# Kernel tuning notes

Hardware: AMD Instinct MI355X
Metric: run time of the kernel (lower is better)

Reference implementation:

```python
import jax, jax.numpy as jnp
import numpy as np

N = 100000
D = 128
E = 1600000
NUM_STEPS = 8
LAM0 = 1.0
LAM1 = 1.0
ALPHA = 1.0 / (1.0 + 0.0 + LAM0 + LAM1)  # args.alp == 0 path


def setup_inputs() -> dict:
    key = jax.random.key(0)
    ks = jax.random.split(key, 12)
    X = jax.random.normal(ks[0], (N, D), dtype=jnp.float32)
    # H init: normal(0, 1/in_features) + I  (notresidual=False branch)
    H1 = jax.random.normal(ks[1], (D, D), dtype=jnp.float32) * (1.0 / D) + jnp.eye(D, dtype=jnp.float32)
    H2 = jax.random.normal(ks[2], (D, D), dtype=jnp.float32) * (1.0 / D) + jnp.eye(D, dtype=jnp.float32)
    w_beta = jax.random.uniform(ks[3], (E,), dtype=jnp.float32)
    w_gamma = jax.random.uniform(ks[4], (E,), dtype=jnp.float32)
    d_beta = jax.random.uniform(ks[5], (N,), dtype=jnp.float32)
    d_gamma = jax.random.uniform(ks[6], (N,), dtype=jnp.float32)
    src_beta = jax.random.randint(ks[7], (E,), 0, N, dtype=jnp.int32)
    dst_beta = jax.random.randint(ks[8], (E,), 0, N, dtype=jnp.int32)
    src_gamma = jax.random.randint(ks[9], (E,), 0, N, dtype=jnp.int32)
    dst_gamma = jax.random.randint(ks[10], (E,), 0, N, dtype=jnp.int32)
    return {"X": X, "H1": H1, "H2": H2, "w_beta": w_beta, "w_gamma": w_gamma,
            "d_beta": d_beta, "d_gamma": d_gamma,
            "src_beta": src_beta, "dst_beta": dst_beta,
            "src_gamma": src_gamma, "dst_gamma": dst_gamma}


def _spmm(w, src, dst, Y):
    # (sparse A) @ Y with A[dst, src] = w
    return jax.ops.segment_sum(w[:, None] * Y[src], dst, num_segments=N)


def reference(X, H1, H2, w_beta, w_gamma, d_beta, d_gamma,
              src_beta, dst_beta, src_gamma, dst_gamma):
    # Q_tild = lam0*D_beta + lam1*D_gamma + I  (diagonal)
    q = LAM0 * d_beta + LAM1 * d_gamma + 1.0  # [N]
    S1 = H1 + H1.T
    P1 = H1 @ H1.T
    S2 = H2 + H2.T
    P2 = H2 @ H2.T
    Y0 = X
    Y = X
    for _ in range(NUM_STEPS):
        AbY = _spmm(w_beta, src_beta, dst_beta, Y)    # A_beta @ Y
        AgY = _spmm(w_gamma, src_gamma, dst_gamma, Y)  # A_gamma @ Y
        term_beta = AbY @ S1 - d_beta[:, None] * (Y @ P1)
        # L_gamma @ Y = D_gamma@Y - A_gamma@Y
        term_gamma = (d_gamma[:, None] * Y - AgY
                      + AgY @ S2 - d_gamma[:, None] * (Y @ P2))
        Y_hat = LAM0 * term_beta + Y0 + LAM1 * term_gamma
        Y = (1.0 - ALPHA) * Y + ALPHA * (Y_hat / q[:, None])
    return Y
```

## Files before the change

kernel.cpp:

```cpp
#include <hip/hip_runtime.h>
#include <cstdint>
#include <cstddef>

#define DD 128
#define ATS 68
#define WTS 130

typedef float f32x8 __attribute__((ext_vector_type(8)));


__global__ void count2_k(const int* __restrict__ dstb, const int* __restrict__ dstg,
                         int* __restrict__ degb, int* __restrict__ degg, int E, int gE) {
    int b = blockIdx.x;
    const int* dst = (b < gE) ? dstb : dstg;
    int* deg = (b < gE) ? degb : degg;
    int i = ((b < gE) ? b : b - gE) * blockDim.x + threadIdx.x;
    if (i < E) atomicAdd(&deg[dst[i]], 1);
}

__global__ __launch_bounds__(1024) void scan2_k(const int* __restrict__ degb,
                                                const int* __restrict__ degg,
                                                int* __restrict__ rpb, int* __restrict__ rpg,
                                                int* __restrict__ curb, int* __restrict__ curg,
                                                int n) {
    const int* deg = (blockIdx.x == 0) ? degb : degg;
    int* rp = (blockIdx.x == 0) ? rpb : rpg;
    int* cur = (blockIdx.x == 0) ? curb : curg;
    __shared__ int sums[1024];
    int tid = threadIdx.x;
    int per = (n + 1023) >> 10;
    int start = tid * per;
    int end = min(start + per, n);
    int s = 0;
    for (int i = start; i < end; ++i) s += deg[i];
    sums[tid] = s;
    __syncthreads();
    for (int off = 1; off < 1024; off <<= 1) {
        int v = (tid >= off) ? sums[tid - off] : 0;
        __syncthreads();
        sums[tid] += v;
        __syncthreads();
    }
    int pre = (tid == 0) ? 0 : sums[tid - 1];
    for (int i = start; i < end; ++i) {
        rp[i] = pre;
        cur[i] = pre;
        pre += deg[i];
    }
    if (end == n) rp[n] = pre;
}

__global__ void fill2_k(const int* __restrict__ srcb, const int* __restrict__ dstb,
                        const float* __restrict__ wb,
                        const int* __restrict__ srcg, const int* __restrict__ dstg,
                        const float* __restrict__ wg,
                        int* __restrict__ curb, int* __restrict__ curg,
                        int2* __restrict__ eb, int2* __restrict__ eg, int E, int gE) {
    int b = blockIdx.x;
    bool isb = (b < gE);
    const int* src = isb ? srcb : srcg;
    const int* dst = isb ? dstb : dstg;
    const float* w = isb ? wb : wg;
    int* cur = isb ? curb : curg;
    int2* edges = isb ? eb : eg;
    int i = (isb ? b : b - gE) * blockDim.x + threadIdx.x;
    if (i < E) {
        int d = dst[i];
        int pos = atomicAdd(&cur[d], 1);
        edges[pos] = make_int2(src[i], __float_as_int(w[i]));
    }
}


__global__ __launch_bounds__(256) void prep_k(const float* __restrict__ H,
                                              float* __restrict__ P,
                                              float* __restrict__ S, int sub_ident) {
    int idx = blockIdx.x * 256 + threadIdx.x;
    int i = idx >> 7, j = idx & 127;
    float acc = 0.f;
    for (int k = 0; k < DD; ++k) acc += H[i * DD + k] * H[j * DD + k];
    P[idx] = acc;
    float s = H[i * DD + j] + H[j * DD + i];
    if (sub_ident && i == j) s -= 1.0f;
    S[idx] = s;
}


__global__ void aq_k(const float* __restrict__ db, const float* __restrict__ dg,
                     float* __restrict__ aq, int n) {
    int i = blockIdx.x * blockDim.x + threadIdx.x;
    if (i < n) aq[i] = (1.0f / 3.0f) / (db[i] + dg[i] + 1.0f);
}


__global__ __launch_bounds__(1024, 2) void denseY_k(
    const float* __restrict__ Yc, const float* __restrict__ X,
    const float* __restrict__ db, const float* __restrict__ dg,
    const float* __restrict__ P1, const float* __restrict__ P2,
    const float* __restrict__ S1, const float* __restrict__ S2m,
    float* __restrict__ YS1, float* __restrict__ YSg, float* __restrict__ R, int n)
{
    __shared__ float At[DD * ATS];

    const int tid  = threadIdx.x;
    const int lane = tid & 63;
    const int wid  = tid >> 6;
    const int cw   = wid << 3;
    const int c0   = __builtin_amdgcn_readfirstlane(cw);
    const int row0 = blockIdx.x * 64;
    const int rowc = min(row0 + lane, n - 1);

    {
        const float* gp = Yc + (size_t)rowc * DD + cw;
        float4 v0 = *reinterpret_cast<const float4*>(gp);
        float4 v1 = *reinterpret_cast<const float4*>(gp + 4);
        At[(cw + 0) * ATS + lane] = v0.x;
        At[(cw + 1) * ATS + lane] = v0.y;
        At[(cw + 2) * ATS + lane] = v0.z;
        At[(cw + 3) * ATS + lane] = v0.w;
        At[(cw + 4) * ATS + lane] = v1.x;
        At[(cw + 5) * ATS + lane] = v1.y;
        At[(cw + 6) * ATS + lane] = v1.z;
        At[(cw + 7) * ATS + lane] = v1.w;
    }
    __syncthreads();

    const float dbv = db[rowc];
    const float dgv = dg[rowc];

    float a1[8], a2[8], aR[8];
    {
        const float* xp = X + (size_t)rowc * DD + cw;
        float4 x0 = *reinterpret_cast<const float4*>(xp);
        float4 x1 = *reinterpret_cast<const float4*>(xp + 4);
        float xv[8] = {x0.x, x0.y, x0.z, x0.w, x1.x, x1.y, x1.z, x1.w};
#pragma unroll
        for (int j = 0; j < 8; ++j) {
            a1[j] = 0.f; a2[j] = 0.f;
            aR[j] = xv[j] + dgv * At[(c0 + j) * ATS + lane];
        }
    }

    {
        const f32x8* pS1 = reinterpret_cast<const f32x8*>(S1 + c0);
        const f32x8* pS2 = reinterpret_cast<const f32x8*>(S2m + c0);
        const f32x8* pP1 = reinterpret_cast<const f32x8*>(P1 + c0);
        const f32x8* pP2 = reinterpret_cast<const f32x8*>(P2 + c0);
#pragma unroll 2
        for (int k = 0; k < DD; ++k) {
            f32x8 b1 = pS1[k * 16];
            f32x8 b2 = pS2[k * 16];
            f32x8 b3 = pP1[k * 16];
            f32x8 b4 = pP2[k * 16];
            float a = At[k * ATS + lane];
            float am1 = dbv * a;
            float am2 = dgv * a;
#pragma unroll
            for (int j = 0; j < 8; ++j) {
                a1[j] += a * b1[j];
                a2[j] += a * b2[j];
                aR[j] -= am1 * b3[j] + am2 * b4[j];
            }
        }
    }

    float* W = At;
    const int r2 = tid >> 4;
    const int c2 = (tid & 15) << 3;
    const int row2 = row0 + r2;

    __syncthreads();
#pragma unroll
    for (int j = 0; j < 8; ++j) W[lane * WTS + cw + j] = a1[j];
    __syncthreads();
    if (row2 < n) {
        float ov[8];
#pragma unroll
        for (int j = 0; j < 8; ++j) ov[j] = W[r2 * WTS + c2 + j];
        float* op = YS1 + (size_t)row2 * DD + c2;
        *reinterpret_cast<float4*>(op) = make_float4(ov[0], ov[1], ov[2], ov[3]);
        *reinterpret_cast<float4*>(op + 4) = make_float4(ov[4], ov[5], ov[6], ov[7]);
    }
    __syncthreads();
#pragma unroll
    for (int j = 0; j < 8; ++j) W[lane * WTS + cw + j] = a2[j];
    __syncthreads();
    if (row2 < n) {
        float ov[8];
#pragma unroll
        for (int j = 0; j < 8; ++j) ov[j] = W[r2 * WTS + c2 + j];
        float* op = YSg + (size_t)row2 * DD + c2;
        *reinterpret_cast<float4*>(op) = make_float4(ov[0], ov[1], ov[2], ov[3]);
        *reinterpret_cast<float4*>(op + 4) = make_float4(ov[4], ov[5], ov[6], ov[7]);
    }
    __syncthreads();
#pragma unroll
    for (int j = 0; j < 8; ++j) W[lane * WTS + cw + j] = aR[j];
    __syncthreads();
    if (row2 < n) {
        float ov[8];
#pragma unroll
        for (int j = 0; j < 8; ++j) ov[j] = W[r2 * WTS + c2 + j];
        float* op = R + (size_t)row2 * DD + c2;
        *reinterpret_cast<float4*>(op) = make_float4(ov[0], ov[1], ov[2], ov[3]);
        *reinterpret_cast<float4*>(op + 4) = make_float4(ov[4], ov[5], ov[6], ov[7]);
    }
}


__global__ __launch_bounds__(256, 8) void spmmF_k(
    const int* __restrict__ rpb, const int2* __restrict__ eb,
    const int* __restrict__ rpg, const int2* __restrict__ eg,
    const float* __restrict__ YS1, const float* __restrict__ YSg,
    const float* __restrict__ Yc, const float* __restrict__ R,
    const float* __restrict__ aq,
    float* __restrict__ Yn, int n)
{
    int node = blockIdx.x * 4 + (threadIdx.x >> 6);
    if (node >= n) return;
    int lane = threadIdx.x & 63;

    int jb = rpb[node], be = rpb[node + 1];
    int jg = rpg[node], ge = rpg[node + 1];
    float b0 = 0.f, b1 = 0.f, g0 = 0.f, g1 = 0.f;

    while (jb + 4 <= be && jg + 4 <= ge) {
        int2 x0 = eb[jb + 0], x1 = eb[jb + 1], x2 = eb[jb + 2], x3 = eb[jb + 3];
        int2 y0 = eg[jg + 0], y1 = eg[jg + 1], y2 = eg[jg + 2], y3 = eg[jg + 3];
        float2 fb0 = *((const float2*)(YS1 + (size_t)x0.x * DD) + lane);
        float2 fb1 = *((const float2*)(YS1 + (size_t)x1.x * DD) + lane);
        float2 fb2 = *((const float2*)(YS1 + (size_t)x2.x * DD) + lane);
        float2 fb3 = *((const float2*)(YS1 + (size_t)x3.x * DD) + lane);
        float2 fg0 = *((const float2*)(YSg + (size_t)y0.x * DD) + lane);
        float2 fg1 = *((const float2*)(YSg + (size_t)y1.x * DD) + lane);
        float2 fg2 = *((const float2*)(YSg + (size_t)y2.x * DD) + lane);
        float2 fg3 = *((const float2*)(YSg + (size_t)y3.x * DD) + lane);
        float wb0 = __int_as_float(x0.y), wb1 = __int_as_float(x1.y);
        float wb2 = __int_as_float(x2.y), wb3 = __int_as_float(x3.y);
        float wg0 = __int_as_float(y0.y), wg1 = __int_as_float(y1.y);
        float wg2 = __int_as_float(y2.y), wg3 = __int_as_float(y3.y);
        b0 += wb0 * fb0.x; b1 += wb0 * fb0.y;
        b0 += wb1 * fb1.x; b1 += wb1 * fb1.y;
        b0 += wb2 * fb2.x; b1 += wb2 * fb2.y;
        b0 += wb3 * fb3.x; b1 += wb3 * fb3.y;
        g0 += wg0 * fg0.x; g1 += wg0 * fg0.y;
        g0 += wg1 * fg1.x; g1 += wg1 * fg1.y;
        g0 += wg2 * fg2.x; g1 += wg2 * fg2.y;
        g0 += wg3 * fg3.x; g1 += wg3 * fg3.y;
        jb += 4; jg += 4;
    }
    while (jb + 4 <= be) {
        int2 x0 = eb[jb + 0], x1 = eb[jb + 1], x2 = eb[jb + 2], x3 = eb[jb + 3];
        float2 f0 = *((const float2*)(YS1 + (size_t)x0.x * DD) + lane);
        float2 f1 = *((const float2*)(YS1 + (size_t)x1.x * DD) + lane);
        float2 f2 = *((const float2*)(YS1 + (size_t)x2.x * DD) + lane);
        float2 f3 = *((const float2*)(YS1 + (size_t)x3.x * DD) + lane);
        float w0 = __int_as_float(x0.y), w1 = __int_as_float(x1.y);
        float w2 = __int_as_float(x2.y), w3 = __int_as_float(x3.y);
        b0 += w0 * f0.x; b1 += w0 * f0.y;
        b0 += w1 * f1.x; b1 += w1 * f1.y;
        b0 += w2 * f2.x; b1 += w2 * f2.y;
        b0 += w3 * f3.x; b1 += w3 * f3.y;
        jb += 4;
    }
    while (jg + 4 <= ge) {
        int2 y0 = eg[jg + 0], y1 = eg[jg + 1], y2 = eg[jg + 2], y3 = eg[jg + 3];
        float2 f0 = *((const float2*)(YSg + (size_t)y0.x * DD) + lane);
        float2 f1 = *((const float2*)(YSg + (size_t)y1.x * DD) + lane);
        float2 f2 = *((const float2*)(YSg + (size_t)y2.x * DD) + lane);
        float2 f3 = *((const float2*)(YSg + (size_t)y3.x * DD) + lane);
        float w0 = __int_as_float(y0.y), w1 = __int_as_float(y1.y);
        float w2 = __int_as_float(y2.y), w3 = __int_as_float(y3.y);
        g0 += w0 * f0.x; g1 += w0 * f0.y;
        g0 += w1 * f1.x; g1 += w1 * f1.y;
        g0 += w2 * f2.x; g1 += w2 * f2.y;
        g0 += w3 * f3.x; g1 += w3 * f3.y;
        jg += 4;
    }
    for (; jb < be; ++jb) {
        int2 e = eb[jb];
        float2 f = *((const float2*)(YS1 + (size_t)e.x * DD) + lane);
        float wv = __int_as_float(e.y);
        b0 += wv * f.x; b1 += wv * f.y;
    }
    for (; jg < ge; ++jg) {
        int2 e = eg[jg];
        float2 f = *((const float2*)(YSg + (size_t)e.x * DD) + lane);
        float wv = __int_as_float(e.y);
        g0 += wv * f.x; g1 += wv * f.y;
    }

    float2 y = *((const float2*)(Yc + (size_t)node * DD) + lane);
    float2 r = *((const float2*)(R + (size_t)node * DD) + lane);
    float aqv = aq[node];
    float2 o;
    o.x = (2.0f / 3.0f) * y.x + (b0 + g0 + r.x) * aqv;
    o.y = (2.0f / 3.0f) * y.y + (b1 + g1 + r.y) * aqv;
    *((float2*)(Yn + (size_t)node * DD) + lane) = o;
}


extern "C" void kernel_launch(void* const* d_in, const int* in_sizes, int n_in,
                              void* d_out, int out_size, void* d_ws, size_t ws_size,
                              hipStream_t stream) {
    const float* X   = (const float*)d_in[0];
    const float* H1  = (const float*)d_in[1];
    const float* H2  = (const float*)d_in[2];
    const float* wb  = (const float*)d_in[3];
    const float* wg  = (const float*)d_in[4];
    const float* db  = (const float*)d_in[5];
    const float* dg  = (const float*)d_in[6];
    const int* srcb  = (const int*)d_in[7];
    const int* dstb  = (const int*)d_in[8];
    const int* srcg  = (const int*)d_in[9];
    const int* dstg  = (const int*)d_in[10];
    const int N = in_sizes[5];
    const int E = in_sizes[3];
    float* Yout = (float*)d_out;

    char* p = (char*)d_ws;
    auto alloc = [&](size_t b) -> void* {
        void* r = (void*)p;
        p += (b + 255) & ~(size_t)255;
        return r;
    };
    float* P1  = (float*)alloc((size_t)DD * DD * 4);
    float* S1  = (float*)alloc((size_t)DD * DD * 4);
    float* P2  = (float*)alloc((size_t)DD * DD * 4);
    float* S2m = (float*)alloc((size_t)DD * DD * 4);
    int* degb = (int*)alloc((size_t)N * 4);
    int* degg = (int*)alloc((size_t)N * 4);
    int* rpb  = (int*)alloc((size_t)(N + 1) * 4);
    int* rpg  = (int*)alloc((size_t)(N + 1) * 4);
    int* curb = (int*)alloc((size_t)N * 4);
    int* curg = (int*)alloc((size_t)N * 4);
    float* aq = (float*)alloc((size_t)N * 4);
    int2* eb  = (int2*)alloc((size_t)E * 8);
    int2* eg  = (int2*)alloc((size_t)E * 8);
    float* YS1 = (float*)alloc((size_t)N * DD * 4);
    float* YSg = (float*)alloc((size_t)N * DD * 4);
    float* R   = (float*)alloc((size_t)N * DD * 4);
    float* Yw  = (float*)alloc((size_t)N * DD * 4);

    hipMemsetAsync(degb, 0, (size_t)N * 4, stream);
    hipMemsetAsync(degg, 0, (size_t)N * 4, stream);

    int gE = (E + 255) / 256;
    count2_k<<<2 * gE, 256, 0, stream>>>(dstb, dstg, degb, degg, E, gE);
    scan2_k<<<2, 1024, 0, stream>>>(degb, degg, rpb, rpg, curb, curg, N);
    fill2_k<<<2 * gE, 256, 0, stream>>>(srcb, dstb, wb, srcg, dstg, wg,
                                        curb, curg, eb, eg, E, gE);
    prep_k<<<64, 256, 0, stream>>>(H1, P1, S1, 0);
    prep_k<<<64, 256, 0, stream>>>(H2, P2, S2m, 1);
    aq_k<<<(N + 255) / 256, 256, 0, stream>>>(db, dg, aq, N);

    const float* Ycur = X;
    float* Ybufs[2] = {Yw, Yout};
    int gs = (N + 3) / 4;
    int gd = (N + 63) / 64;
    for (int s = 0; s < 8; ++s) {
        float* Yn = Ybufs[s & 1];
        denseY_k<<<gd, 1024, 0, stream>>>(Ycur, X, db, dg, P1, P2, S1, S2m,
                                          YS1, YSg, R, N);
        spmmF_k<<<gs, 256, 0, stream>>>(rpb, eb, rpg, eg, YS1, YSg,
                                        Ycur, R, aq, Yn, N);
        Ycur = Yn;
    }
}
```

Baseline: 4.200 ms.

## Reassociate sparse-dense products and co-schedule gather with dense transform in one kernel

Each step now computes A_beta@Y and A_gamma@Y by gathering directly from Y, then applies S1/S2 afterwards, instead of transforming Y by S1/S2 first and gathering those results. The first kernel interleaves sparse gather blocks with dense blocks that compute the P1/P2 residual, so memory-bound gather work can overlap ALU-heavy dense work. A second kernel applies S1/S2 to the aggregated rows and writes the step output. Both gathers now read one shared Y array, which shrinks the cache working set. The cost is extra global traffic for the AbY/AgY intermediates, one more full dense pass, and dense loads that are now strided per lane without LDS staging.

```diff
diff --git a/kernel.cpp b/kernel.cpp
--- a/kernel.cpp
+++ b/kernel.cpp
@@ -3,8 +3,6 @@
 #include <cstddef>
 
 #define DD 128
-#define ATS 68
-#define WTS 130
 
 typedef float f32x8 __attribute__((ext_vector_type(8)));
 
@@ -85,7 +83,6 @@
     S[idx] = s;
 }
 
-
 __global__ void aq_k(const float* __restrict__ db, const float* __restrict__ dg,
                      float* __restrict__ aq, int n) {
     int i = blockIdx.x * blockDim.x + threadIdx.x;
@@ -93,210 +90,203 @@
 }
 
 
-__global__ __launch_bounds__(1024, 2) void denseY_k(
+__global__ __launch_bounds__(256, 8) void k1_mix(
     const float* __restrict__ Yc, const float* __restrict__ X,
+    const int* __restrict__ rpb, const int2* __restrict__ eb,
+    const int* __restrict__ rpg, const int2* __restrict__ eg,
     const float* __restrict__ db, const float* __restrict__ dg,
     const float* __restrict__ P1, const float* __restrict__ P2,
-    const float* __restrict__ S1, const float* __restrict__ S2m,
-    float* __restrict__ YS1, float* __restrict__ YSg, float* __restrict__ R, int n)
+    float* __restrict__ AbY, float* __restrict__ AgY, float* __restrict__ R,
+    int n, int ndense)
 {
-    __shared__ float At[DD * ATS];
-
-    const int tid  = threadIdx.x;
+    const int bid = blockIdx.x;
+    const int tid = threadIdx.x;
+    const int r5 = bid % 5;
+
+    if (r5 != 4) {
+        int sid = (bid / 5) * 4 + r5;
+        int node = sid * 4 + (tid >> 6);
+        if (node >= n) return;
+        int lane = tid & 63;
+
+        int jb = rpb[node], be = rpb[node + 1];
+        int jg = rpg[node], ge = rpg[node + 1];
+        float b0 = 0.f, b1 = 0.f, g0 = 0.f, g1 = 0.f;
+
+        while (jb + 4 <= be && jg + 4 <= ge) {
+            int2 x0 = eb[jb + 0], x1 = eb[jb + 1], x2 = eb[jb + 2], x3 = eb[jb + 3];
+            int2 y0 = eg[jg + 0], y1 = eg[jg + 1], y2 = eg[jg + 2], y3 = eg[jg + 3];
+            float2 fb0 = *((const float2*)(Yc + (size_t)x0.x * DD) + lane);
+            float2 fb1 = *((const float2*)(Yc + (size_t)x1.x * DD) + lane);
+            float2 fb2 = *((const float2*)(Yc + (size_t)x2.x * DD) + lane);
+            float2 fb3 = *((const float2*)(Yc + (size_t)x3.x * DD) + lane);
+            float2 fg0 = *((const float2*)(Yc + (size_t)y0.x * DD) + lane);
+            float2 fg1 = *((const float2*)(Yc + (size_t)y1.x * DD) + lane);
+            float2 fg2 = *((const float2*)(Yc + (size_t)y2.x * DD) + lane);
+            float2 fg3 = *((const float2*)(Yc + (size_t)y3.x * DD) + lane);
+            float wb0 = __int_as_float(x0.y), wb1 = __int_as_float(x1.y);
+            float wb2 = __int_as_float(x2.y), wb3 = __int_as_float(x3.y);
+            float wg0 = __int_as_float(y0.y), wg1 = __int_as_float(y1.y);
+            float wg2 = __int_as_float(y2.y), wg3 = __int_as_float(y3.y);
+            b0 += wb0 * fb0.x; b1 += wb0 * fb0.y;
+            b0 += wb1 * fb1.x; b1 += wb1 * fb1.y;
+            b0 += wb2 * fb2.x; b1 += wb2 * fb2.y;
+            b0 += wb3 * fb3.x; b1 += wb3 * fb3.y;
+            g0 += wg0 * fg0.x; g1 += wg0 * fg0.y;
+            g0 += wg1 * fg1.x; g1 += wg1 * fg1.y;
+            g0 += wg2 * fg2.x; g1 += wg2 * fg2.y;
+            g0 += wg3 * fg3.x; g1 += wg3 * fg3.y;
+            jb += 4; jg += 4;
+        }
+        while (jb + 4 <= be) {
+            int2 x0 = eb[jb + 0], x1 = eb[jb + 1], x2 = eb[jb + 2], x3 = eb[jb + 3];
+            float2 f0 = *((const float2*)(Yc + (size_t)x0.x * DD) + lane);
+            float2 f1 = *((const float2*)(Yc + (size_t)x1.x * DD) + lane);
+            float2 f2 = *((const float2*)(Yc + (size_t)x2.x * DD) + lane);
+            float2 f3 = *((const float2*)(Yc + (size_t)x3.x * DD) + lane);
+            float w0 = __int_as_float(x0.y), w1 = __int_as_float(x1.y);
+            float w2 = __int_as_float(x2.y), w3 = __int_as_float(x3.y);
+            b0 += w0 * f0.x; b1 += w0 * f0.y;
+            b0 += w1 * f1.x; b1 += w1 * f1.y;
+            b0 += w2 * f2.x; b1 += w2 * f2.y;
+            b0 += w3 * f3.x; b1 += w3 * f3.y;
+            jb += 4;
+        }
+        while (jg + 4 <= ge) {
+            int2 y0 = eg[jg + 0], y1 = eg[jg + 1], y2 = eg[jg + 2], y3 = eg[jg + 3];
+            float2 f0 = *((const float2*)(Yc + (size_t)y0.x * DD) + lane);
+            float2 f1 = *((const float2*)(Yc + (size_t)y1.x * DD) + lane);
+            float2 f2 = *((const float2*)(Yc + (size_t)y2.x * DD) + lane);
+            float2 f3 = *((const float2*)(Yc + (size_t)y3.x * DD) + lane);
+            float w0 = __int_as_float(y0.y), w1 = __int_as_float(y1.y);
+            float w2 = __int_as_float(y2.y), w3 = __int_as_float(y3.y);
+            g0 += w0 * f0.x; g1 += w0 * f0.y;
+            g0 += w1 * f1.x; g1 += w1 * f1.y;
+            g0 += w2 * f2.x; g1 += w2 * f2.y;
+            g0 += w3 * f3.x; g1 += w3 * f3.y;
+            jg += 4;
+        }
+        for (; jb < be; ++jb) {
+            int2 e = eb[jb];
+            float2 f = *((const float2*)(Yc + (size_t)e.x * DD) + lane);
+            float wv = __int_as_float(e.y);
+            b0 += wv * f.x; b1 += wv * f.y;
+        }
+        for (; jg < ge; ++jg) {
+            int2 e = eg[jg];
+            float2 f = *((const float2*)(Yc + (size_t)e.x * DD) + lane);
+            float wv = __int_as_float(e.y);
+            g0 += wv * f.x; g1 += wv * f.y;
+        }
+        *((float2*)(AbY + (size_t)node * DD) + lane) = make_float2(b0, b1);
+        *((float2*)(AgY + (size_t)node * DD) + lane) = make_float2(g0, g1);
+        return;
+    }
+
+    int did = bid / 5;
+    if (did >= ndense) return;
+    const int row0 = (did >> 2) * 64;
+    const int cs = did & 3;
     const int lane = tid & 63;
-    const int wid  = tid >> 6;
-    const int cw   = wid << 3;
-    const int c0   = __builtin_amdgcn_readfirstlane(cw);
-    const int row0 = blockIdx.x * 64;
+    const int w = tid >> 6;
+    const int cw = cs * 32 + w * 8;
+    const int c0 = __builtin_amdgcn_readfirstlane(cw);
     const int rowc = min(row0 + lane, n - 1);
-
-    {
-        const float* gp = Yc + (size_t)rowc * DD + cw;
-        float4 v0 = *reinterpret_cast<const float4*>(gp);
-        float4 v1 = *reinterpret_cast<const float4*>(gp + 4);
-        At[(cw + 0) * ATS + lane] = v0.x;
-        At[(cw + 1) * ATS + lane] = v0.y;
-        At[(cw + 2) * ATS + lane] = v0.z;
-        At[(cw + 3) * ATS + lane] = v0.w;
-        At[(cw + 4) * ATS + lane] = v1.x;
-        At[(cw + 5) * ATS + lane] = v1.y;
-        At[(cw + 6) * ATS + lane] = v1.z;
-        At[(cw + 7) * ATS + lane] = v1.w;
-    }
-    __syncthreads();
 
     const float dbv = db[rowc];
     const float dgv = dg[rowc];
-
-    float a1[8], a2[8], aR[8];
+    const float* yrow = Yc + (size_t)rowc * DD;
+
+    float aR[8];
     {
-        const float* xp = X + (size_t)rowc * DD + cw;
-        float4 x0 = *reinterpret_cast<const float4*>(xp);
-        float4 x1 = *reinterpret_cast<const float4*>(xp + 4);
-        float xv[8] = {x0.x, x0.y, x0.z, x0.w, x1.x, x1.y, x1.z, x1.w};
-#pragma unroll
-        for (int j = 0; j < 8; ++j) {
-            a1[j] = 0.f; a2[j] = 0.f;
-            aR[j] = xv[j] + dgv * At[(c0 + j) * ATS + lane];
-        }
-    }
-
-    {
-        const f32x8* pS1 = reinterpret_cast<const f32x8*>(S1 + c0);
-        const f32x8* pS2 = reinterpret_cast<const f32x8*>(S2m + c0);
-        const f32x8* pP1 = reinterpret_cast<const f32x8*>(P1 + c0);
-        const f32x8* pP2 = reinterpret_cast<const f32x8*>(P2 + c0);
+        const float* xp = X + (size_t)rowc * DD + c0;
+        const float* yp = yrow + c0;
+#pragma unroll
+        for (int j = 0; j < 8; ++j) aR[j] = xp[j] + dgv * yp[j];
+    }
+
+    const f32x8* pP1 = reinterpret_cast<const f32x8*>(P1 + c0);
+    const f32x8* pP2 = reinterpret_cast<const f32x8*>(P2 + c0);
 #pragma unroll 2
-        for (int k = 0; k < DD; ++k) {
-            f32x8 b1 = pS1[k * 16];
-            f32x8 b2 = pS2[k * 16];
-            f32x8 b3 = pP1[k * 16];
-            f32x8 b4 = pP2[k * 16];
-            float a = At[k * ATS + lane];
+    for (int kc = 0; kc < 16; ++kc) {
+        f32x8 ych = *reinterpret_cast<const f32x8*>(yrow + kc * 8);
+#pragma unroll
+        for (int t = 0; t < 8; ++t) {
+            int k = kc * 8 + t;
+            float a = ych[t];
             float am1 = dbv * a;
             float am2 = dgv * a;
-#pragma unroll
-            for (int j = 0; j < 8; ++j) {
-                a1[j] += a * b1[j];
-                a2[j] += a * b2[j];
-                aR[j] -= am1 * b3[j] + am2 * b4[j];
-            }
-        }
-    }
-
-    float* W = At;
-    const int r2 = tid >> 4;
-    const int c2 = (tid & 15) << 3;
-    const int row2 = row0 + r2;
-
-    __syncthreads();
-#pragma unroll
-    for (int j = 0; j < 8; ++j) W[lane * WTS + cw + j] = a1[j];
-    __syncthreads();
-    if (row2 < n) {
+            f32x8 r1 = pP1[k * 16];
+            f32x8 r2 = pP2[k * 16];
+#pragma unroll
+            for (int j = 0; j < 8; ++j) aR[j] -= am1 * r1[j] + am2 * r2[j];
+        }
+    }
+
+    if (row0 + lane < n) {
+        float* op = R + (size_t)rowc * DD + c0;
+        *reinterpret_cast<float4*>(op) = make_float4(aR[0], aR[1], aR[2], aR[3]);
+        *reinterpret_cast<float4*>(op + 4) = make_float4(aR[4], aR[5], aR[6], aR[7]);
+    }
+}
+
+
+__global__ __launch_bounds__(256, 8) void k2_denseS(
+    const float* __restrict__ Yc,
+    const float* __restrict__ AbY, const float* __restrict__ AgY,
+    const float* __restrict__ R, const float* __restrict__ aq,
+    const float* __restrict__ S1, const float* __restrict__ S2m,
+    float* __restrict__ Yn, int n)
+{
+    const int did = blockIdx.x;
+    const int row0 = (did >> 2) * 64;
+    const int cs = did & 3;
+    const int tid = threadIdx.x;
+    const int lane = tid & 63;
+    const int w = tid >> 6;
+    const int cw = cs * 32 + w * 8;
+    const int c0 = __builtin_amdgcn_readfirstlane(cw);
+    const int rowc = min(row0 + lane, n - 1);
+
+    const float* brow = AbY + (size_t)rowc * DD;
+    const float* grow = AgY + (size_t)rowc * DD;
+
+    float acc[8];
+    {
+        const float* rp_ = R + (size_t)rowc * DD + c0;
+#pragma unroll
+        for (int j = 0; j < 8; ++j) acc[j] = rp_[j];
+    }
+
+    const f32x8* pS1 = reinterpret_cast<const f32x8*>(S1 + c0);
+    const f32x8* pS2 = reinterpret_cast<const f32x8*>(S2m + c0);
+#pragma unroll 2
+    for (int kc = 0; kc < 16; ++kc) {
+        f32x8 bch = *reinterpret_cast<const f32x8*>(brow + kc * 8);
+        f32x8 gch = *reinterpret_cast<const f32x8*>(grow + kc * 8);
+#pragma unroll
+        for (int t = 0; t < 8; ++t) {
+            int k = kc * 8 + t;
+            float a1 = bch[t];
+            float a2 = gch[t];
+            f32x8 r1 = pS1[k * 16];
+            f32x8 r2 = pS2[k * 16];
+#pragma unroll
+            for (int j = 0; j < 8; ++j) acc[j] += a1 * r1[j] + a2 * r2[j];
+        }
+    }
+
+    if (row0 + lane < n) {
+        const float aqv = aq[rowc];
+        const float* yp = Yc + (size_t)rowc * DD + c0;
         float ov[8];
 #pragma unroll
-        for (int j = 0; j < 8; ++j) ov[j] = W[r2 * WTS + c2 + j];
-        float* op = YS1 + (size_t)row2 * DD + c2;
+        for (int j = 0; j < 8; ++j)
+            ov[j] = (2.0f / 3.0f) * yp[j] + acc[j] * aqv;
+        float* op = Yn + (size_t)rowc * DD + c0;
         *reinterpret_cast<float4*>(op) = make_float4(ov[0], ov[1], ov[2], ov[3]);
         *reinterpret_cast<float4*>(op + 4) = make_float4(ov[4], ov[5], ov[6], ov[7]);
     }
-    __syncthreads();
-#pragma unroll
-    for (int j = 0; j < 8; ++j) W[lane * WTS + cw + j] = a2[j];
-    __syncthreads();
-    if (row2 < n) {
-        float ov[8];
-#pragma unroll
-        for (int j = 0; j < 8; ++j) ov[j] = W[r2 * WTS + c2 + j];
-        float* op = YSg + (size_t)row2 * DD + c2;
-        *reinterpret_cast<float4*>(op) = make_float4(ov[0], ov[1], ov[2], ov[3]);
-        *reinterpret_cast<float4*>(op + 4) = make_float4(ov[4], ov[5], ov[6], ov[7]);
-    }
-    __syncthreads();
-#pragma unroll
-    for (int j = 0; j < 8; ++j) W[lane * WTS + cw + j] = aR[j];
-    __syncthreads();
-    if (row2 < n) {
-        float ov[8];
-#pragma unroll
-        for (int j = 0; j < 8; ++j) ov[j] = W[r2 * WTS + c2 + j];
-        float* op = R + (size_t)row2 * DD + c2;
-        *reinterpret_cast<float4*>(op) = make_float4(ov[0], ov[1], ov[2], ov[3]);
-        *reinterpret_cast<float4*>(op + 4) = make_float4(ov[4], ov[5], ov[6], ov[7]);
-    }
-}
-
-
-__global__ __launch_bounds__(256, 8) void spmmF_k(
-    const int* __restrict__ rpb, const int2* __restrict__ eb,
-    const int* __restrict__ rpg, const int2* __restrict__ eg,
-    const float* __restrict__ YS1, const float* __restrict__ YSg,
-    const float* __restrict__ Yc, const float* __restrict__ R,
-    const float* __restrict__ aq,
-    float* __restrict__ Yn, int n)
-{
-    int node = blockIdx.x * 4 + (threadIdx.x >> 6);
-    if (node >= n) return;
-    int lane = threadIdx.x & 63;
-
-    int jb = rpb[node], be = rpb[node + 1];
-    int jg = rpg[node], ge = rpg[node + 1];
-    float b0 = 0.f, b1 = 0.f, g0 = 0.f, g1 = 0.f;
-
-    while (jb + 4 <= be && jg + 4 <= ge) {
-        int2 x0 = eb[jb + 0], x1 = eb[jb + 1], x2 = eb[jb + 2], x3 = eb[jb + 3];
-        int2 y0 = eg[jg + 0], y1 = eg[jg + 1], y2 = eg[jg + 2], y3 = eg[jg + 3];
-        float2 fb0 = *((const float2*)(YS1 + (size_t)x0.x * DD) + lane);
-        float2 fb1 = *((const float2*)(YS1 + (size_t)x1.x * DD) + lane);
-        float2 fb2 = *((const float2*)(YS1 + (size_t)x2.x * DD) + lane);
-        float2 fb3 = *((const float2*)(YS1 + (size_t)x3.x * DD) + lane);
-        float2 fg0 = *((const float2*)(YSg + (size_t)y0.x * DD) + lane);
-        float2 fg1 = *((const float2*)(YSg + (size_t)y1.x * DD) + lane);
-        float2 fg2 = *((const float2*)(YSg + (size_t)y2.x * DD) + lane);
-        float2 fg3 = *((const float2*)(YSg + (size_t)y3.x * DD) + lane);
-        float wb0 = __int_as_float(x0.y), wb1 = __int_as_float(x1.y);
-        float wb2 = __int_as_float(x2.y), wb3 = __int_as_float(x3.y);
-        float wg0 = __int_as_float(y0.y), wg1 = __int_as_float(y1.y);
-        float wg2 = __int_as_float(y2.y), wg3 = __int_as_float(y3.y);
-        b0 += wb0 * fb0.x; b1 += wb0 * fb0.y;
-        b0 += wb1 * fb1.x; b1 += wb1 * fb1.y;
-        b0 += wb2 * fb2.x; b1 += wb2 * fb2.y;
-        b0 += wb3 * fb3.x; b1 += wb3 * fb3.y;
-        g0 += wg0 * fg0.x; g1 += wg0 * fg0.y;
-        g0 += wg1 * fg1.x; g1 += wg1 * fg1.y;
-        g0 += wg2 * fg2.x; g1 += wg2 * fg2.y;
-        g0 += wg3 * fg3.x; g1 += wg3 * fg3.y;
-        jb += 4; jg += 4;
-    }
-    while (jb + 4 <= be) {
-        int2 x0 = eb[jb + 0], x1 = eb[jb + 1], x2 = eb[jb + 2], x3 = eb[jb + 3];
-        float2 f0 = *((const float2*)(YS1 + (size_t)x0.x * DD) + lane);
-        float2 f1 = *((const float2*)(YS1 + (size_t)x1.x * DD) + lane);
-        float2 f2 = *((const float2*)(YS1 + (size_t)x2.x * DD) + lane);
-        float2 f3 = *((const float2*)(YS1 + (size_t)x3.x * DD) + lane);
-        float w0 = __int_as_float(x0.y), w1 = __int_as_float(x1.y);
-        float w2 = __int_as_float(x2.y), w3 = __int_as_float(x3.y);
-        b0 += w0 * f0.x; b1 += w0 * f0.y;
-        b0 += w1 * f1.x; b1 += w1 * f1.y;
-        b0 += w2 * f2.x; b1 += w2 * f2.y;
-        b0 += w3 * f3.x; b1 += w3 * f3.y;
-        jb += 4;
-    }
-    while (jg + 4 <= ge) {
-        int2 y0 = eg[jg + 0], y1 = eg[jg + 1], y2 = eg[jg + 2], y3 = eg[jg + 3];
-        float2 f0 = *((const float2*)(YSg + (size_t)y0.x * DD) + lane);
-        float2 f1 = *((const float2*)(YSg + (size_t)y1.x * DD) + lane);
-        float2 f2 = *((const float2*)(YSg + (size_t)y2.x * DD) + lane);
-        float2 f3 = *((const float2*)(YSg + (size_t)y3.x * DD) + lane);
-        float w0 = __int_as_float(y0.y), w1 = __int_as_float(y1.y);
-        float w2 = __int_as_float(y2.y), w3 = __int_as_float(y3.y);
-        g0 += w0 * f0.x; g1 += w0 * f0.y;
-        g0 += w1 * f1.x; g1 += w1 * f1.y;
-        g0 += w2 * f2.x; g1 += w2 * f2.y;
-        g0 += w3 * f3.x; g1 += w3 * f3.y;
-        jg += 4;
-    }
-    for (; jb < be; ++jb) {
-        int2 e = eb[jb];
-        float2 f = *((const float2*)(YS1 + (size_t)e.x * DD) + lane);
-        float wv = __int_as_float(e.y);
-        b0 += wv * f.x; b1 += wv * f.y;
-    }
-    for (; jg < ge; ++jg) {
-        int2 e = eg[jg];
-        float2 f = *((const float2*)(YSg + (size_t)e.x * DD) + lane);
-        float wv = __int_as_float(e.y);
-        g0 += wv * f.x; g1 += wv * f.y;
-    }
-
-    float2 y = *((const float2*)(Yc + (size_t)node * DD) + lane);
-    float2 r = *((const float2*)(R + (size_t)node * DD) + lane);
-    float aqv = aq[node];
-    float2 o;
-    o.x = (2.0f / 3.0f) * y.x + (b0 + g0 + r.x) * aqv;
-    o.y = (2.0f / 3.0f) * y.y + (b1 + g1 + r.y) * aqv;
-    *((float2*)(Yn + (size_t)node * DD) + lane) = o;
 }
 
 
@@ -337,8 +327,8 @@
     float* aq = (float*)alloc((size_t)N * 4);
     int2* eb  = (int2*)alloc((size_t)E * 8);
     int2* eg  = (int2*)alloc((size_t)E * 8);
-    float* YS1 = (float*)alloc((size_t)N * DD * 4);
-    float* YSg = (float*)alloc((size_t)N * DD * 4);
+    float* AbY = (float*)alloc((size_t)N * DD * 4);
+    float* AgY = (float*)alloc((size_t)N * DD * 4);
     float* R   = (float*)alloc((size_t)N * DD * 4);
     float* Yw  = (float*)alloc((size_t)N * DD * 4);
 
@@ -356,14 +346,15 @@
 
     const float* Ycur = X;
     float* Ybufs[2] = {Yw, Yout};
-    int gs = (N + 3) / 4;
     int gd = (N + 63) / 64;
+    int ND = gd * 4;
+    int T = 5 * ND;
     for (int s = 0; s < 8; ++s) {
         float* Yn = Ybufs[s & 1];
-        denseY_k<<<gd, 1024, 0, stream>>>(Ycur, X, db, dg, P1, P2, S1, S2m,
-                                          YS1, YSg, R, N);
-        spmmF_k<<<gs, 256, 0, stream>>>(rpb, eb, rpg, eg, YS1, YSg,
-                                        Ycur, R, aq, Yn, N);
+        k1_mix<<<T, 256, 0, stream>>>(Ycur, X, rpb, eb, rpg, eg, db, dg,
+                                      P1, P2, AbY, AgY, R, N, ND);
+        k2_denseS<<<ND, 256, 0, stream>>>(Ycur, AbY, AgY, R, aq,
+                                          S1, S2m, Yn, N);
         Ycur = Yn;
     }
 }
```

Result: slower. 6.521 ms (+55.3%).
